# Optimization experiments

Hardware: AMD Instinct MI355X
Metric: run time of the kernel (lower is better)

Reference implementation:

```python
import jax, jax.numpy as jnp
import numpy as np

N_HEADS = 4
M = 16            # n_points (neighbors kept per voxel)
DIST = 4          # manhattan distance threshold
D_MODEL = 128
D_FFN = 256
D_CHL = 64
GRID = 96         # spatial_shape per axis
LN_EPS = 1e-5
BN_EPS = 1e-3


def setup_inputs() -> dict:
    key = jax.random.key(0)
    ks = jax.random.split(key, 24)
    N = 8192
    w = lambda k, s: jax.random.normal(k, s, jnp.float32) * 0.02
    z = lambda d: jnp.zeros((d,), jnp.float32)
    o = lambda d: jnp.ones((d,), jnp.float32)
    return {
        "features": jax.random.normal(ks[0], (N, D_CHL), jnp.float32),
        "coords": jax.random.randint(ks[1], (N, 3), 0, GRID, jnp.int32),
        "pe_w1": w(ks[2], (3, D_MODEL // 2)), "pe_b1": z(D_MODEL // 2),
        "pe_w2": w(ks[3], (D_MODEL // 2, D_MODEL)), "pe_b2": z(D_MODEL),
        "in_w": w(ks[4], (D_CHL, D_MODEL)), "in_b": z(D_MODEL),
        "q_w": w(ks[5], (D_MODEL, D_MODEL)), "q_b": z(D_MODEL),
        "k_w": w(ks[6], (D_MODEL, D_MODEL)), "k_b": z(D_MODEL),
        "v_w": w(ks[7], (D_MODEL, D_MODEL)), "v_b": z(D_MODEL),
        "o_w": w(ks[8], (D_MODEL, D_MODEL)), "o_b": z(D_MODEL),
        "n1_g": o(D_MODEL), "n1_b": z(D_MODEL),
        "l1_w": w(ks[9], (D_MODEL, D_FFN)), "l1_b": z(D_FFN),
        "l2_w": w(ks[10], (D_FFN, D_MODEL)), "l2_b": z(D_MODEL),
        "n3_g": o(D_MODEL), "n3_b": z(D_MODEL),
        "fu_w": w(ks[11], (D_MODEL + D_CHL, D_CHL)), "fu_b": z(D_CHL),
        "bn_g": o(D_CHL), "bn_b": z(D_CHL),
    }


def _layernorm(x, g, b):
    mu = jnp.mean(x, -1, keepdims=True)
    var = jnp.mean(jnp.square(x - mu), -1, keepdims=True)
    return (x - mu) * jax.lax.rsqrt(var + LN_EPS) * g + b


def reference(features, coords, pe_w1, pe_b1, pe_w2, pe_b2, in_w, in_b,
              q_w, q_b, k_w, k_b, v_w, v_b, o_w, o_b, n1_g, n1_b,
              l1_w, l1_b, l2_w, l2_b, n3_g, n3_b, fu_w, fu_b, bn_g, bn_b):
    N = features.shape[0]
    hd = D_MODEL // N_HEADS
    ci = coords.astype(jnp.float32)
    # input projection + dynamic learnable positional encoding
    src = features @ in_w + in_b
    vc = ci / (GRID - 1.0)
    src = src + (jax.nn.relu(vc @ pe_w1 + pe_b1) @ pe_w2 + pe_b2)
    # pairwise manhattan distances; accumulate per coordinate to avoid [N,N,3]
    dist = jnp.zeros((N, N), jnp.float32)
    for d in range(3):
        dist = dist + jnp.abs(ci[:, d, None] - ci[None, :, d])
    dist = jnp.where(dist <= DIST, dist, jnp.inf)
    neg_top, idx = jax.lax.top_k(-dist, M)          # [N, M]
    valid = neg_top != -jnp.inf
    # gather neighbor features; invalid slots are zero (as in torch)
    nb = jnp.where(valid[:, :, None], src[jnp.where(valid, idx, 0)], 0.0)  # [N,M,D]
    # cross-attention: query is neighbor 0 (self). NOTE: faithful raw .view
    # reshape of [N,M,D] -> [N,H,M,hd] (interleaves neighbor/head axes as torch does)
    q = (nb[:, :1] @ q_w + q_b).reshape(N, N_HEADS, 1, hd)
    k = (nb @ k_w + k_b).reshape(N, N_HEADS, M, hd)
    v = (nb @ v_w + v_b).reshape(N, N_HEADS, M, hd)
    scores = jnp.einsum('nhqd,nhkd->nhqk', q, k) / jnp.sqrt(jnp.float32(D_MODEL))
    attn = jax.nn.softmax(scores, axis=-1)
    head_out = jnp.einsum('nhqk,nhkd->nhqd', attn, v).reshape(N, D_MODEL)
    out = head_out @ o_w + o_b
    tgt = _layernorm(src + out, n1_g, n1_b)
    # FFN
    tgt2 = jax.nn.relu(tgt @ l1_w + l1_b) @ l2_w + l2_b
    tgt = _layernorm(tgt + tgt2, n3_g, n3_b)
    # EnhancedFusion: concat -> linear -> batchnorm (train-mode stats) -> relu
    fused = jnp.concatenate([features, tgt], axis=1) @ fu_w + fu_b
    mu = jnp.mean(fused, 0)
    var = jnp.var(fused, 0)
    fused = (fused - mu) * jax.lax.rsqrt(var + BN_EPS) * bn_g + bn_b
    return jax.nn.relu(fused)
```

## Files before the change

### kernel.cpp

```cpp
#include <hip/hip_runtime.h>

#define DEVFN __device__ __forceinline__

DEVFN float relu(float x) { return x < 0.f ? 0.f : x; }

__global__ void k0_zero_cst(float* __restrict__ p, int n)
{
    int i = blockIdx.x * 256 + threadIdx.x;
    if (i < n) p[i] = 0.f;
}

__global__ __launch_bounds__(256) void k1_src_cst(
    const float* __restrict__ features, const int* __restrict__ coords,
    const float* __restrict__ pe_w1, const float* __restrict__ pe_b1,
    const float* __restrict__ pe_w2, const float* __restrict__ pe_b2,
    const float* __restrict__ in_w, const float* __restrict__ in_b,
    float* __restrict__ src, int* __restrict__ packed)
{
    __shared__ float sF[512];
    __shared__ float sH[512];
    __shared__ int   sC[24];
    const int tid = threadIdx.x;
    const int r0 = blockIdx.x * 8;
    if (tid < 24) sC[tid] = coords[r0 * 3 + tid];
    for (int i = tid; i < 512; i += 256) sF[i] = features[r0 * 64 + i];
    __syncthreads();
    for (int i = tid; i < 512; i += 256) {
        int r = i >> 6, t = i & 63;
        float v0 = sC[r * 3 + 0] * (1.f / 95.f);
        float v1 = sC[r * 3 + 1] * (1.f / 95.f);
        float v2 = sC[r * 3 + 2] * (1.f / 95.f);
        float h = v0 * pe_w1[t] + v1 * pe_w1[64 + t] + v2 * pe_w1[128 + t] + pe_b1[t];
        sH[i] = relu(h);
    }
    __syncthreads();
    const int c = tid & 127, rh = tid >> 7;
    float acc[4];
    const float base = in_b[c] + pe_b2[c];
#pragma unroll
    for (int r = 0; r < 4; ++r) acc[r] = base;
    for (int j = 0; j < 64; ++j) {
        float w1 = in_w[j * 128 + c];
        float w2 = pe_w2[j * 128 + c];
#pragma unroll
        for (int r = 0; r < 4; ++r) {
            int rr = rh * 4 + r;
            acc[r] += sF[rr * 64 + j] * w1 + sH[rr * 64 + j] * w2;
        }
    }
#pragma unroll
    for (int r = 0; r < 4; ++r) src[(r0 + rh * 4 + r) * 128 + c] = acc[r];
    if (tid < 8)
        packed[r0 + tid] = sC[tid * 3] | (sC[tid * 3 + 1] << 8) | (sC[tid * 3 + 2] << 16);
}

__global__ __launch_bounds__(256) void k2_nbr_cst(
    const int* __restrict__ packed, int* __restrict__ nbr, int N)
{
    __shared__ int pc[8192];
    __shared__ int cnt[16];
    __shared__ int lst[16 * 64];
    __shared__ int outL[256];
    const int tid = threadIdx.x;
    for (int i = tid; i < N; i += 256) pc[i] = packed[i];
    if (tid < 16) cnt[tid] = 0;
    outL[tid] = -1;
    __syncthreads();
    const int q0 = blockIdx.x * 16;
    int qx[16], qy[16], qz[16];
#pragma unroll
    for (int q = 0; q < 16; ++q) {
        int p = pc[q0 + q];
        qx[q] = p & 255; qy[q] = (p >> 8) & 255; qz[q] = p >> 16;
    }
    for (int cd = tid; cd < N; cd += 256) {
        int p = pc[cd];
        int cx = p & 255, cy = (p >> 8) & 255, cz = p >> 16;
#pragma unroll
        for (int q = 0; q < 16; ++q) {
            int dx = cx - qx[q]; dx = dx < 0 ? -dx : dx;
            int dy = cy - qy[q]; dy = dy < 0 ? -dy : dy;
            int dz = cz - qz[q]; dz = dz < 0 ? -dz : dz;
            int d = dx + dy + dz;
            if (d <= 4) {
                int s = atomicAdd(&cnt[q], 1);
                if (s < 64) lst[q * 64 + s] = (d << 13) | cd;
            }
        }
    }
    __syncthreads();
    {
        const int q = tid >> 4, t = tid & 15;
        int n = cnt[q]; if (n > 64) n = 64;
        for (int e = t; e < n; e += 16) {
            int key = lst[q * 64 + e];
            int rank = 0;
            for (int j = 0; j < n; ++j) rank += (lst[q * 64 + j] < key) ? 1 : 0;
            if (rank < 16) outL[q * 16 + rank] = key & 8191;
        }
    }
    __syncthreads();
    {
        const int q = tid >> 4, t = tid & 15;
        nbr[(q0 + q) * 16 + t] = outL[q * 16 + t];
    }
}

__global__ __launch_bounds__(256) void k3_qkv_cst(
    const float* __restrict__ src,
    const float* __restrict__ q_w, const float* __restrict__ k_w,
    const float* __restrict__ v_w,
    float* __restrict__ qs, float* __restrict__ ks, float* __restrict__ vs)
{
    __shared__ float S[1024];
    const int tid = threadIdx.x;
    const int r0 = blockIdx.x * 8;
    const int which = blockIdx.y;
    const float* __restrict__ w = (which == 0) ? q_w : (which == 1) ? k_w : v_w;
    float* __restrict__ out = (which == 0) ? qs : (which == 1) ? ks : vs;
    for (int i = tid; i < 1024; i += 256) S[i] = src[r0 * 128 + i];
    __syncthreads();
    const int c = tid & 127, rh = tid >> 7;
    float acc[4];
#pragma unroll
    for (int r = 0; r < 4; ++r) acc[r] = 0.f;
    for (int k4 = 0; k4 < 32; ++k4) {
        float w0 = w[(k4 * 4 + 0) * 128 + c];
        float w1 = w[(k4 * 4 + 1) * 128 + c];
        float w2 = w[(k4 * 4 + 2) * 128 + c];
        float w3 = w[(k4 * 4 + 3) * 128 + c];
#pragma unroll
        for (int r = 0; r < 4; ++r) {
            float4 s = *(const float4*)(&S[(rh * 4 + r) * 128 + k4 * 4]);
            acc[r] += s.x * w0 + s.y * w1 + s.z * w2 + s.w * w3;
        }
    }
#pragma unroll
    for (int r = 0; r < 4; ++r) out[(r0 + rh * 4 + r) * 128 + c] = acc[r];
}

DEVFN void ln_rows8(float* Cb, const float* __restrict__ g,
                    const float* __restrict__ b, int tid)
{
    const int r = tid >> 5, l = tid & 31;
    float x[4]; float s = 0.f, s2 = 0.f;
#pragma unroll
    for (int i = 0; i < 4; ++i) {
        x[i] = Cb[r * 128 + l * 4 + i];
        s += x[i]; s2 += x[i] * x[i];
    }
#pragma unroll
    for (int o = 1; o < 32; o <<= 1) { s += __shfl_xor(s, o); s2 += __shfl_xor(s2, o); }
    float mu = s * (1.f / 128.f);
    float var = s2 * (1.f / 128.f) - mu * mu;
    float rstd = rsqrtf(var + 1e-5f);
#pragma unroll
    for (int i = 0; i < 4; ++i) {
        int cc = l * 4 + i;
        Cb[r * 128 + cc] = (x[i] - mu) * rstd * g[cc] + b[cc];
    }
}

__global__ __launch_bounds__(256) void k4_main_cst(
    const float* __restrict__ features, const float* __restrict__ src,
    const float* __restrict__ qs, const float* __restrict__ ks, const float* __restrict__ vs,
    const int* __restrict__ nbr,
    const float* __restrict__ q_b, const float* __restrict__ k_b,
    const float* __restrict__ v_b,
    const float* __restrict__ o_w, const float* __restrict__ o_b,
    const float* __restrict__ n1_g, const float* __restrict__ n1_b,
    const float* __restrict__ l1_w, const float* __restrict__ l1_b,
    const float* __restrict__ l2_w, const float* __restrict__ l2_b,
    const float* __restrict__ n3_g, const float* __restrict__ n3_b,
    const float* __restrict__ fu_w, const float* __restrict__ fu_b,
    float* __restrict__ fused, float* __restrict__ bnSum, float* __restrict__ bnSq)
{
    __shared__ float A[1024];
    __shared__ float Bt[1024];
    __shared__ float C[1024];
    __shared__ float Q[1024];
    __shared__ float H[2048];
    __shared__ float SC[512];
    __shared__ float F[512];
    __shared__ __align__(16) float bK[128], bV[128];
    __shared__ float bQ[128];
    __shared__ int idxL[128];
    const int tid = threadIdx.x;
    const int r0 = blockIdx.x * 8;

    for (int i = tid; i < 1024; i += 256) A[i] = src[r0 * 128 + i];
    for (int i = tid; i < 512; i += 256) F[i] = features[r0 * 64 + i];
    if (tid < 128) {
        idxL[tid] = nbr[r0 * 16 + tid];
        bQ[tid] = q_b[tid]; bK[tid] = k_b[tid]; bV[tid] = v_b[tid];
    }
    __syncthreads();
    for (int i = tid; i < 1024; i += 256) {
        int r = i >> 7, c = i & 127;
        int i0 = idxL[r * 16];
        Q[i] = (i0 < 0 ? 0.f : qs[i0 * 128 + c]) + bQ[c];
    }
    __syncthreads();

    const int ar = tid >> 5, ah = (tid >> 3) & 3, ag = tid & 7;
    {
#pragma unroll
        for (int jj = 0; jj < 2; ++jj) {
            int j = ag + jj * 8;
            int j4 = j >> 2, ch = j & 3;
            int id = idxL[ar * 16 + ah * 4 + j4];
            float s = 0.f;
#pragma unroll
            for (int c4 = 0; c4 < 8; ++c4) {
                float4 qv = *(const float4*)(&Q[ar * 128 + ah * 32 + c4 * 4]);
                float4 kb = *(const float4*)(&bK[ch * 32 + c4 * 4]);
                float4 kv = make_float4(0.f, 0.f, 0.f, 0.f);
                if (id >= 0) kv = *(const float4*)(ks + id * 128 + ch * 32 + c4 * 4);
                s += qv.x * (kv.x + kb.x) + qv.y * (kv.y + kb.y)
                   + qv.z * (kv.z + kb.z) + qv.w * (kv.w + kb.w);
            }
            SC[ar * 64 + ah * 16 + j] = s * 0.08838834764831845f;
        }
    }
    __syncthreads();

    {
        float p[16];
        float mx = -3.4e38f;
#pragma unroll
        for (int j = 0; j < 16; ++j) { p[j] = SC[ar * 64 + ah * 16 + j]; mx = fmaxf(mx, p[j]); }
        float sum = 0.f;
#pragma unroll
        for (int j = 0; j < 16; ++j) { p[j] = __expf(p[j] - mx); sum += p[j]; }
        float inv = 1.f / sum;
        float4 acc = make_float4(0.f, 0.f, 0.f, 0.f);
#pragma unroll
        for (int j = 0; j < 16; ++j) {
            int j4 = j >> 2, ch = j & 3;
            int id = idxL[ar * 16 + ah * 4 + j4];
            float4 vb = *(const float4*)(&bV[ch * 32 + ag * 4]);
            float4 vv = make_float4(0.f, 0.f, 0.f, 0.f);
            if (id >= 0) vv = *(const float4*)(vs + id * 128 + ch * 32 + ag * 4);
            float w = p[j] * inv;
            acc.x += w * (vv.x + vb.x); acc.y += w * (vv.y + vb.y);
            acc.z += w * (vv.z + vb.z); acc.w += w * (vv.w + vb.w);
        }
        *(float4*)(&Bt[ar * 128 + ah * 32 + ag * 4]) = acc;
    }
    __syncthreads();

    {
        const int c = tid & 127, rh = tid >> 7;
        float acc[4];
        const float ob = o_b[c];
#pragma unroll
        for (int r = 0; r < 4; ++r) acc[r] = ob;
        for (int k4 = 0; k4 < 32; ++k4) {
            float w0 = o_w[(k4 * 4 + 0) * 128 + c];
            float w1 = o_w[(k4 * 4 + 1) * 128 + c];
            float w2 = o_w[(k4 * 4 + 2) * 128 + c];
            float w3 = o_w[(k4 * 4 + 3) * 128 + c];
#pragma unroll
            for (int r = 0; r < 4; ++r) {
                float4 t = *(const float4*)(&Bt[(rh * 4 + r) * 128 + k4 * 4]);
                acc[r] += t.x * w0 + t.y * w1 + t.z * w2 + t.w * w3;
            }
        }
#pragma unroll
        for (int r = 0; r < 4; ++r) {
            int row = rh * 4 + r;
            C[row * 128 + c] = A[row * 128 + c] + acc[r];
        }
    }
    __syncthreads();
    ln_rows8(C, n1_g, n1_b, tid);
    __syncthreads();

    {
        const int f = tid;
        float acc[8];
#pragma unroll
        for (int r = 0; r < 8; ++r) acc[r] = 0.f;
        for (int k4 = 0; k4 < 32; ++k4) {
            float w0 = l1_w[(k4 * 4 + 0) * 256 + f];
            float w1 = l1_w[(k4 * 4 + 1) * 256 + f];
            float w2 = l1_w[(k4 * 4 + 2) * 256 + f];
            float w3 = l1_w[(k4 * 4 + 3) * 256 + f];
#pragma unroll
            for (int r = 0; r < 8; ++r) {
                float4 t = *(const float4*)(&C[r * 128 + k4 * 4]);
                acc[r] += t.x * w0 + t.y * w1 + t.z * w2 + t.w * w3;
            }
        }
        const float bb = l1_b[f];
#pragma unroll
        for (int r = 0; r < 8; ++r) H[r * 256 + f] = relu(acc[r] + bb);
    }
    __syncthreads();

    {
        const int c = tid & 127, rh = tid >> 7;
        float acc[4];
        const float lb = l2_b[c];
#pragma unroll
        for (int r = 0; r < 4; ++r) acc[r] = lb;
        for (int k4 = 0; k4 < 64; ++k4) {
            float w0 = l2_w[(k4 * 4 + 0) * 128 + c];
            float w1 = l2_w[(k4 * 4 + 1) * 128 + c];
            float w2 = l2_w[(k4 * 4 + 2) * 128 + c];
            float w3 = l2_w[(k4 * 4 + 3) * 128 + c];
#pragma unroll
            for (int r = 0; r < 4; ++r) {
                float4 t = *(const float4*)(&H[(rh * 4 + r) * 256 + k4 * 4]);
                acc[r] += t.x * w0 + t.y * w1 + t.z * w2 + t.w * w3;
            }
        }
#pragma unroll
        for (int r = 0; r < 4; ++r) {
            int row = rh * 4 + r;
            C[row * 128 + c] += acc[r];
        }
    }
    __syncthreads();
    ln_rows8(C, n3_g, n3_b, tid);
    __syncthreads();

    {
        const int c = tid & 63, rg = tid >> 6;
        float acc[2];
        const float fb = fu_b[c];
#pragma unroll
        for (int r = 0; r < 2; ++r) acc[r] = fb;
        for (int j4 = 0; j4 < 16; ++j4) {
            float w0 = fu_w[(j4 * 4 + 0) * 64 + c];
            float w1 = fu_w[(j4 * 4 + 1) * 64 + c];
            float w2 = fu_w[(j4 * 4 + 2) * 64 + c];
            float w3 = fu_w[(j4 * 4 + 3) * 64 + c];
#pragma unroll
            for (int r = 0; r < 2; ++r) {
                float4 t = *(const float4*)(&F[(rg * 2 + r) * 64 + j4 * 4]);
                acc[r] += t.x * w0 + t.y * w1 + t.z * w2 + t.w * w3;
            }
        }
        for (int j4 = 0; j4 < 32; ++j4) {
            float w0 = fu_w[(64 + j4 * 4 + 0) * 64 + c];
            float w1 = fu_w[(64 + j4 * 4 + 1) * 64 + c];
            float w2 = fu_w[(64 + j4 * 4 + 2) * 64 + c];
            float w3 = fu_w[(64 + j4 * 4 + 3) * 64 + c];
#pragma unroll
            for (int r = 0; r < 2; ++r) {
                float4 t = *(const float4*)(&C[(rg * 2 + r) * 128 + j4 * 4]);
                acc[r] += t.x * w0 + t.y * w1 + t.z * w2 + t.w * w3;
            }
        }
#pragma unroll
        for (int r = 0; r < 2; ++r) {
            int row = rg * 2 + r;
            float v = acc[r];
            fused[(r0 + row) * 64 + c] = v;
            H[row * 64 + c] = v;
        }
    }
    __syncthreads();
    if (tid < 64) {
        float s = 0.f, s2 = 0.f;
#pragma unroll
        for (int r = 0; r < 8; ++r) { float x = H[r * 64 + tid]; s += x; s2 += x * x; }
        atomicAdd(&bnSum[tid], s);
        atomicAdd(&bnSq[tid], s2);
    }
}

__global__ __launch_bounds__(256) void k5_bn_cst(
    const float* __restrict__ fused, const float* __restrict__ bnSum,
    const float* __restrict__ bnSq,
    const float* __restrict__ g, const float* __restrict__ b,
    float* __restrict__ out, int N)
{
    const int total = N * 64;
    const float invN = 1.f / (float)N;
    for (int i = blockIdx.x * 256 + threadIdx.x; i < total; i += gridDim.x * 256) {
        int c = i & 63;
        float mu = bnSum[c] * invN;
        float var = bnSq[c] * invN - mu * mu;
        float x = fused[i];
        float y = (x - mu) * rsqrtf(var + 1e-3f) * g[c] + b[c];
        out[i] = relu(y);
    }
}

extern "C" void kernel_launch(void* const* d_in, const int* in_sizes, int n_in,
                              void* d_out, int out_size, void* d_ws, size_t ws_size,
                              hipStream_t stream)
{
    const float* features = (const float*)d_in[0];
    const int*   coords   = (const int*)d_in[1];
    const float* pe_w1 = (const float*)d_in[2];
    const float* pe_b1 = (const float*)d_in[3];
    const float* pe_w2 = (const float*)d_in[4];
    const float* pe_b2 = (const float*)d_in[5];
    const float* in_w  = (const float*)d_in[6];
    const float* in_b  = (const float*)d_in[7];
    const float* q_w   = (const float*)d_in[8];
    const float* q_b   = (const float*)d_in[9];
    const float* k_w   = (const float*)d_in[10];
    const float* k_b   = (const float*)d_in[11];
    const float* v_w   = (const float*)d_in[12];
    const float* v_b   = (const float*)d_in[13];
    const float* o_w   = (const float*)d_in[14];
    const float* o_b   = (const float*)d_in[15];
    const float* n1_g  = (const float*)d_in[16];
    const float* n1_b  = (const float*)d_in[17];
    const float* l1_w  = (const float*)d_in[18];
    const float* l1_b  = (const float*)d_in[19];
    const float* l2_w  = (const float*)d_in[20];
    const float* l2_b  = (const float*)d_in[21];
    const float* n3_g  = (const float*)d_in[22];
    const float* n3_b  = (const float*)d_in[23];
    const float* fu_w  = (const float*)d_in[24];
    const float* fu_b  = (const float*)d_in[25];
    const float* bn_g  = (const float*)d_in[26];
    const float* bn_b  = (const float*)d_in[27];

    const int N = in_sizes[0] / 64;

    float* src   = (float*)d_ws;
    float* qs    = src + (size_t)N * 128;
    float* ks    = qs  + (size_t)N * 128;
    float* vs    = ks  + (size_t)N * 128;
    float* fused = vs  + (size_t)N * 128;
    int*   packed = (int*)(fused + (size_t)N * 64);
    int*   nbr    = packed + N;
    float* bnSum  = (float*)(nbr + (size_t)N * 16);
    float* bnSq   = bnSum + 64;

    k0_zero_cst<<<1, 256, 0, stream>>>(bnSum, 128);
    k1_src_cst<<<N / 8, 256, 0, stream>>>(features, coords, pe_w1, pe_b1, pe_w2, pe_b2,
                                          in_w, in_b, src, packed);
    k2_nbr_cst<<<N / 16, 256, 0, stream>>>(packed, nbr, N);
    k3_qkv_cst<<<dim3(N / 8, 3), 256, 0, stream>>>(src, q_w, k_w, v_w, qs, ks, vs);
    k4_main_cst<<<N / 8, 256, 0, stream>>>(features, src, qs, ks, vs, nbr,
                                           q_b, k_b, v_b, o_w, o_b, n1_g, n1_b,
                                           l1_w, l1_b, l2_w, l2_b, n3_g, n3_b,
                                           fu_w, fu_b, fused, bnSum, bnSq);
    k5_bn_cst<<<512, 256, 0, stream>>>(fused, bnSum, bnSq, bn_g, bn_b,
                                       (float*)d_out, N);
}
```

Before: 235.9 us.

## Fuse src projection with QKV projection and fold BN zeroing into neighbor kernel

Merges the input/positional-encoding projection kernel with the Q/K/V projection kernel, so src stays in shared memory and is not reloaded from global memory. The separate zeroing kernel for the batch-norm accumulators is removed, and that zeroing now happens in block 0 of the neighbor-search kernel. Weight-loop pointers are hoisted and loops are given unroll-4 pragmas throughout. Together these cut two launches and one global round-trip of src. In exchange, the fused kernel does three times the per-block work with only N/8 blocks, where QKV previously used a 3x grid, which lowers parallelism.

```diff
diff --git a/kernel.cpp b/kernel.cpp
--- a/kernel.cpp
+++ b/kernel.cpp
@@ -4,21 +4,19 @@
 
 DEVFN float relu(float x) { return x < 0.f ? 0.f : x; }
 
-__global__ void k0_zero_cst(float* __restrict__ p, int n)
-{
-    int i = blockIdx.x * 256 + threadIdx.x;
-    if (i < n) p[i] = 0.f;
-}
-
-__global__ __launch_bounds__(256) void k1_src_cst(
+__global__ __launch_bounds__(256) void k13_src_qkv_cst(
     const float* __restrict__ features, const int* __restrict__ coords,
     const float* __restrict__ pe_w1, const float* __restrict__ pe_b1,
     const float* __restrict__ pe_w2, const float* __restrict__ pe_b2,
     const float* __restrict__ in_w, const float* __restrict__ in_b,
-    float* __restrict__ src, int* __restrict__ packed)
+    const float* __restrict__ q_w, const float* __restrict__ k_w,
+    const float* __restrict__ v_w,
+    float* __restrict__ src, int* __restrict__ packed,
+    float* __restrict__ qs, float* __restrict__ ks, float* __restrict__ vs)
 {
     __shared__ float sF[512];
     __shared__ float sH[512];
+    __shared__ float S[1024];
     __shared__ int   sC[24];
     const int tid = threadIdx.x;
     const int r0 = blockIdx.x * 8;
@@ -35,33 +33,67 @@
     }
     __syncthreads();
     const int c = tid & 127, rh = tid >> 7;
-    float acc[4];
-    const float base = in_b[c] + pe_b2[c];
-#pragma unroll
-    for (int r = 0; r < 4; ++r) acc[r] = base;
-    for (int j = 0; j < 64; ++j) {
-        float w1 = in_w[j * 128 + c];
-        float w2 = pe_w2[j * 128 + c];
+    {
+        float acc[4];
+        const float base = in_b[c] + pe_b2[c];
+#pragma unroll
+        for (int r = 0; r < 4; ++r) acc[r] = base;
+        const float* w1p = in_w + c;
+        const float* w2p = pe_w2 + c;
+#pragma unroll 4
+        for (int j = 0; j < 64; ++j) {
+            float w1 = w1p[j * 128];
+            float w2 = w2p[j * 128];
+#pragma unroll
+            for (int r = 0; r < 4; ++r) {
+                int rr = rh * 4 + r;
+                acc[r] += sF[rr * 64 + j] * w1 + sH[rr * 64 + j] * w2;
+            }
+        }
 #pragma unroll
         for (int r = 0; r < 4; ++r) {
-            int rr = rh * 4 + r;
-            acc[r] += sF[rr * 64 + j] * w1 + sH[rr * 64 + j] * w2;
-        }
-    }
-#pragma unroll
-    for (int r = 0; r < 4; ++r) src[(r0 + rh * 4 + r) * 128 + c] = acc[r];
-    if (tid < 8)
-        packed[r0 + tid] = sC[tid * 3] | (sC[tid * 3 + 1] << 8) | (sC[tid * 3 + 2] << 16);
+            src[(r0 + rh * 4 + r) * 128 + c] = acc[r];
+            S[(rh * 4 + r) * 128 + c] = acc[r];
+        }
+        if (tid < 8)
+            packed[r0 + tid] = sC[tid * 3] | (sC[tid * 3 + 1] << 8) | (sC[tid * 3 + 2] << 16);
+    }
+    __syncthreads();
+#pragma unroll
+    for (int which = 0; which < 3; ++which) {
+        const float* __restrict__ w = (which == 0) ? q_w : (which == 1) ? k_w : v_w;
+        float* __restrict__ out = (which == 0) ? qs : (which == 1) ? ks : vs;
+        float acc[4];
+#pragma unroll
+        for (int r = 0; r < 4; ++r) acc[r] = 0.f;
+        const float* wp = w + c;
+#pragma unroll 4
+        for (int k4 = 0; k4 < 32; ++k4) {
+            float w0 = wp[(k4 * 4 + 0) * 128];
+            float w1 = wp[(k4 * 4 + 1) * 128];
+            float w2 = wp[(k4 * 4 + 2) * 128];
+            float w3 = wp[(k4 * 4 + 3) * 128];
+#pragma unroll
+            for (int r = 0; r < 4; ++r) {
+                float4 s = *(const float4*)(&S[(rh * 4 + r) * 128 + k4 * 4]);
+                acc[r] += s.x * w0 + s.y * w1 + s.z * w2 + s.w * w3;
+            }
+        }
+#pragma unroll
+        for (int r = 0; r < 4; ++r) out[(r0 + rh * 4 + r) * 128 + c] = acc[r];
+    }
 }
 
 __global__ __launch_bounds__(256) void k2_nbr_cst(
-    const int* __restrict__ packed, int* __restrict__ nbr, int N)
+    const int* __restrict__ packed, int* __restrict__ nbr,
+    float* __restrict__ bnAcc, int N)
 {
     __shared__ int pc[8192];
     __shared__ int cnt[16];
     __shared__ int lst[16 * 64];
     __shared__ int outL[256];
     const int tid = threadIdx.x;
+    if (blockIdx.x == 0 && tid < 128) bnAcc[tid] = 0.f;
     for (int i = tid; i < N; i += 256) pc[i] = packed[i];
     if (tid < 16) cnt[tid] = 0;
     outL[tid] = -1;
@@ -104,39 +136,6 @@
         const int q = tid >> 4, t = tid & 15;
         nbr[(q0 + q) * 16 + t] = outL[q * 16 + t];
     }
-}
-
-__global__ __launch_bounds__(256) void k3_qkv_cst(
-    const float* __restrict__ src,
-    const float* __restrict__ q_w, const float* __restrict__ k_w,
-    const float* __restrict__ v_w,
-    float* __restrict__ qs, float* __restrict__ ks, float* __restrict__ vs)
-{
-    __shared__ float S[1024];
-    const int tid = threadIdx.x;
-    const int r0 = blockIdx.x * 8;
-    const int which = blockIdx.y;
-    const float* __restrict__ w = (which == 0) ? q_w : (which == 1) ? k_w : v_w;
-    float* __restrict__ out = (which == 0) ? qs : (which == 1) ? ks : vs;
-    for (int i = tid; i < 1024; i += 256) S[i] = src[r0 * 128 + i];
-    __syncthreads();
-    const int c = tid & 127, rh = tid >> 7;
-    float acc[4];
-#pragma unroll
-    for (int r = 0; r < 4; ++r) acc[r] = 0.f;
-    for (int k4 = 0; k4 < 32; ++k4) {
-        float w0 = w[(k4 * 4 + 0) * 128 + c];
-        float w1 = w[(k4 * 4 + 1) * 128 + c];
-        float w2 = w[(k4 * 4 + 2) * 128 + c];
-        float w3 = w[(k4 * 4 + 3) * 128 + c];
-#pragma unroll
-        for (int r = 0; r < 4; ++r) {
-            float4 s = *(const float4*)(&S[(rh * 4 + r) * 128 + k4 * 4]);
-            acc[r] += s.x * w0 + s.y * w1 + s.z * w2 + s.w * w3;
-        }
-    }
-#pragma unroll
-    for (int r = 0; r < 4; ++r) out[(r0 + rh * 4 + r) * 128 + c] = acc[r];
 }
 
 DEVFN void ln_rows8(float* Cb, const float* __restrict__ g,
@@ -255,11 +254,13 @@
         const float ob = o_b[c];
 #pragma unroll
         for (int r = 0; r < 4; ++r) acc[r] = ob;
+        const float* wp = o_w + c;
+#pragma unroll 4
         for (int k4 = 0; k4 < 32; ++k4) {
-            float w0 = o_w[(k4 * 4 + 0) * 128 + c];
-            float w1 = o_w[(k4 * 4 + 1) * 128 + c];
-            float w2 = o_w[(k4 * 4 + 2) * 128 + c];
-            float w3 = o_w[(k4 * 4 + 3) * 128 + c];
+            float w0 = wp[(k4 * 4 + 0) * 128];
+            float w1 = wp[(k4 * 4 + 1) * 128];
+            float w2 = wp[(k4 * 4 + 2) * 128];
+            float w3 = wp[(k4 * 4 + 3) * 128];
 #pragma unroll
             for (int r = 0; r < 4; ++r) {
                 float4 t = *(const float4*)(&Bt[(rh * 4 + r) * 128 + k4 * 4]);
@@ -281,11 +282,13 @@
         float acc[8];
 #pragma unroll
         for (int r = 0; r < 8; ++r) acc[r] = 0.f;
+        const float* wp = l1_w + f;
+#pragma unroll 4
         for (int k4 = 0; k4 < 32; ++k4) {
-            float w0 = l1_w[(k4 * 4 + 0) * 256 + f];
-            float w1 = l1_w[(k4 * 4 + 1) * 256 + f];
-            float w2 = l1_w[(k4 * 4 + 2) * 256 + f];
-            float w3 = l1_w[(k4 * 4 + 3) * 256 + f];
+            float w0 = wp[(k4 * 4 + 0) * 256];
+            float w1 = wp[(k4 * 4 + 1) * 256];
+            float w2 = wp[(k4 * 4 + 2) * 256];
+            float w3 = wp[(k4 * 4 + 3) * 256];
 #pragma unroll
             for (int r = 0; r < 8; ++r) {
                 float4 t = *(const float4*)(&C[r * 128 + k4 * 4]);
@@ -304,11 +307,13 @@
         const float lb = l2_b[c];
 #pragma unroll
         for (int r = 0; r < 4; ++r) acc[r] = lb;
+        const float* wp = l2_w + c;
+#pragma unroll 4
         for (int k4 = 0; k4 < 64; ++k4) {
-            float w0 = l2_w[(k4 * 4 + 0) * 128 + c];
-            float w1 = l2_w[(k4 * 4 + 1) * 128 + c];
-            float w2 = l2_w[(k4 * 4 + 2) * 128 + c];
-            float w3 = l2_w[(k4 * 4 + 3) * 128 + c];
+            float w0 = wp[(k4 * 4 + 0) * 128];
+            float w1 = wp[(k4 * 4 + 1) * 128];
+            float w2 = wp[(k4 * 4 + 2) * 128];
+            float w3 = wp[(k4 * 4 + 3) * 128];
 #pragma unroll
             for (int r = 0; r < 4; ++r) {
                 float4 t = *(const float4*)(&H[(rh * 4 + r) * 256 + k4 * 4]);
@@ -331,22 +336,26 @@
         const float fb = fu_b[c];
 #pragma unroll
         for (int r = 0; r < 2; ++r) acc[r] = fb;
+        const float* wp = fu_w + c;
+#pragma unroll 4
         for (int j4 = 0; j4 < 16; ++j4) {
-            float w0 = fu_w[(j4 * 4 + 0) * 64 + c];
-            float w1 = fu_w[(j4 * 4 + 1) * 64 + c];
-            float w2 = fu_w[(j4 * 4 + 2) * 64 + c];
-            float w3 = fu_w[(j4 * 4 + 3) * 64 + c];
+            float w0 = wp[(j4 * 4 + 0) * 64];
+            float w1 = wp[(j4 * 4 + 1) * 64];
+            float w2 = wp[(j4 * 4 + 2) * 64];
+            float w3 = wp[(j4 * 4 + 3) * 64];
 #pragma unroll
             for (int r = 0; r < 2; ++r) {
                 float4 t = *(const float4*)(&F[(rg * 2 + r) * 64 + j4 * 4]);
                 acc[r] += t.x * w0 + t.y * w1 + t.z * w2 + t.w * w3;
             }
         }
+        const float* wp2 = fu_w + 64 * 64 + c;
+#pragma unroll 4
         for (int j4 = 0; j4 < 32; ++j4) {
-            float w0 = fu_w[(64 + j4 * 4 + 0) * 64 + c];
-            float w1 = fu_w[(64 + j4 * 4 + 1) * 64 + c];
-            float w2 = fu_w[(64 + j4 * 4 + 2) * 64 + c];
-            float w3 = fu_w[(64 + j4 * 4 + 3) * 64 + c];
+            float w0 = wp2[(j4 * 4 + 0) * 64];
+            float w1 = wp2[(j4 * 4 + 1) * 64];
+            float w2 = wp2[(j4 * 4 + 2) * 64];
+            float w3 = wp2[(j4 * 4 + 3) * 64];
 #pragma unroll
             for (int r = 0; r < 2; ++r) {
                 float4 t = *(const float4*)(&C[(rg * 2 + r) * 128 + j4 * 4]);
@@ -434,11 +443,11 @@
     float* bnSum  = (float*)(nbr + (size_t)N * 16);
     float* bnSq   = bnSum + 64;
 
-    k0_zero_cst<<<1, 256, 0, stream>>>(bnSum, 128);
-    k1_src_cst<<<N / 8, 256, 0, stream>>>(features, coords, pe_w1, pe_b1, pe_w2, pe_b2,
-                                          in_w, in_b, src, packed);
-    k2_nbr_cst<<<N / 16, 256, 0, stream>>>(packed, nbr, N);
-    k3_qkv_cst<<<dim3(N / 8, 3), 256, 0, stream>>>(src, q_w, k_w, v_w, qs, ks, vs);
+    k13_src_qkv_cst<<<N / 8, 256, 0, stream>>>(features, coords, pe_w1, pe_b1,
+                                               pe_w2, pe_b2, in_w, in_b,
+                                               q_w, k_w, v_w,
+                                               src, packed, qs, ks, vs);
+    k2_nbr_cst<<<N / 16, 256, 0, stream>>>(packed, nbr, bnSum, N);
     k4_main_cst<<<N / 8, 256, 0, stream>>>(features, src, qs, ks, vs, nbr,
                                            q_b, k_b, v_b, o_w, o_b, n1_g, n1_b,
                                            l1_w, l1_b, l2_w, l2_b, n3_g, n3_b,
```

After: 242.8 us. +2.9%, slower.

## Fuse src projection, QKV, neighbor search and BN zeroing into one kernel

Applied to the files above, without the earlier changes.

Merges the zeroing kernel, the src/positional-encoding kernel, the neighbor search kernel and the QKV projection into one launch. Src blocks and neighbor-search blocks run side by side, split by block index. The neighbor search now reads coords straight from global memory instead of staging packed coords in 32KB of LDS. QKV is computed from src kept in shared memory, which removes the src re-read and three separate launches. The cost is a larger LDS footprint per block across both roles, more registers for the three accumulators, and uncoalesced strided coord reads in the search loop.

```diff
diff --git a/kernel.cpp b/kernel.cpp
--- a/kernel.cpp
+++ b/kernel.cpp
@@ -4,23 +4,77 @@
 
 DEVFN float relu(float x) { return x < 0.f ? 0.f : x; }
 
-__global__ void k0_zero_cst(float* __restrict__ p, int n)
-{
-    int i = blockIdx.x * 256 + threadIdx.x;
-    if (i < n) p[i] = 0.f;
-}
-
-__global__ __launch_bounds__(256) void k1_src_cst(
+__global__ __launch_bounds__(256) void ka_pre_cst(
     const float* __restrict__ features, const int* __restrict__ coords,
     const float* __restrict__ pe_w1, const float* __restrict__ pe_b1,
     const float* __restrict__ pe_w2, const float* __restrict__ pe_b2,
     const float* __restrict__ in_w, const float* __restrict__ in_b,
-    float* __restrict__ src, int* __restrict__ packed)
+    const float* __restrict__ q_w, const float* __restrict__ k_w,
+    const float* __restrict__ v_w,
+    float* __restrict__ src,
+    float* __restrict__ qs, float* __restrict__ ks, float* __restrict__ vs,
+    int* __restrict__ nbr, float* __restrict__ bnAcc, int N)
 {
     __shared__ float sF[512];
     __shared__ float sH[512];
+    __shared__ float S[1024];
     __shared__ int   sC[24];
+    __shared__ int cnt[16];
+    __shared__ int lst[16 * 64];
+    __shared__ int outL[256];
+
     const int tid = threadIdx.x;
+    const int nSrcBlocks = N / 8;
+
+    if ((int)blockIdx.x >= nSrcBlocks) {
+        const int nb = blockIdx.x - nSrcBlocks;
+        const int q0 = nb * 16;
+        if (nb == 0 && tid < 128) bnAcc[tid] = 0.f;
+        if (tid < 16) cnt[tid] = 0;
+        outL[tid] = -1;
+        __syncthreads();
+        int qx[16], qy[16], qz[16];
+#pragma unroll
+        for (int q = 0; q < 16; ++q) {
+            qx[q] = coords[(q0 + q) * 3 + 0];
+            qy[q] = coords[(q0 + q) * 3 + 1];
+            qz[q] = coords[(q0 + q) * 3 + 2];
+        }
+        for (int cd = tid; cd < N; cd += 256) {
+            int cx = coords[cd * 3 + 0];
+            int cy = coords[cd * 3 + 1];
+            int cz = coords[cd * 3 + 2];
+#pragma unroll
+            for (int q = 0; q < 16; ++q) {
+                int dx = cx - qx[q]; dx = dx < 0 ? -dx : dx;
+                int dy = cy - qy[q]; dy = dy < 0 ? -dy : dy;
+                int dz = cz - qz[q]; dz = dz < 0 ? -dz : dz;
+                int d = dx + dy + dz;
+                if (d <= 4) {
+                    int s = atomicAdd(&cnt[q], 1);
+                    if (s < 64) lst[q * 64 + s] = (d << 13) | cd;
+                }
+            }
+        }
+        __syncthreads();
+        {
+            const int q = tid >> 4, t = tid & 15;
+            int n = cnt[q]; if (n > 64) n = 64;
+            for (int e = t; e < n; e += 16) {
+                int key = lst[q * 64 + e];
+                int rank = 0;
+                for (int j = 0; j < n; ++j) rank += (lst[q * 64 + j] < key) ? 1 : 0;
+                if (rank < 16) outL[q * 16 + rank] = key & 8191;
+            }
+        }
+        __syncthreads();
+        {
+            const int q = tid >> 4, t = tid & 15;
+            nbr[(q0 + q) * 16 + t] = outL[q * 16 + t];
+        }
+        return;
+    }
+
     const int r0 = blockIdx.x * 8;
     if (tid < 24) sC[tid] = coords[r0 * 3 + tid];
     for (int i = tid; i < 512; i += 256) sF[i] = features[r0 * 64 + i];
@@ -35,108 +89,59 @@
     }
     __syncthreads();
     const int c = tid & 127, rh = tid >> 7;
-    float acc[4];
-    const float base = in_b[c] + pe_b2[c];
-#pragma unroll
-    for (int r = 0; r < 4; ++r) acc[r] = base;
-    for (int j = 0; j < 64; ++j) {
-        float w1 = in_w[j * 128 + c];
-        float w2 = pe_w2[j * 128 + c];
+    {
+        float acc[4];
+        const float base = in_b[c] + pe_b2[c];
+#pragma unroll
+        for (int r = 0; r < 4; ++r) acc[r] = base;
+        for (int j = 0; j < 64; ++j) {
+            float w1 = in_w[j * 128 + c];
+            float w2 = pe_w2[j * 128 + c];
+#pragma unroll
+            for (int r = 0; r < 4; ++r) {
+                int rr = rh * 4 + r;
+                acc[r] += sF[rr * 64 + j] * w1 + sH[rr * 64 + j] * w2;
+            }
+        }
 #pragma unroll
         for (int r = 0; r < 4; ++r) {
-            int rr = rh * 4 + r;
-            acc[r] += sF[rr * 64 + j] * w1 + sH[rr * 64 + j] * w2;
-        }
-    }
-#pragma unroll
-    for (int r = 0; r < 4; ++r) src[(r0 + rh * 4 + r) * 128 + c] = acc[r];
-    if (tid < 8)
-        packed[r0 + tid] = sC[tid * 3] | (sC[tid * 3 + 1] << 8) | (sC[tid * 3 + 2] << 16);
-}
-
-__global__ __launch_bounds__(256) void k2_nbr_cst(
-    const int* __restrict__ packed, int* __restrict__ nbr, int N)
-{
-    __shared__ int pc[8192];
-    __shared__ int cnt[16];
-    __shared__ int lst[16 * 64];
-    __shared__ int outL[256];
-    const int tid = threadIdx.x;
-    for (int i = tid; i < N; i += 256) pc[i] = packed[i];
-    if (tid < 16) cnt[tid] = 0;
-    outL[tid] = -1;
-    __syncthreads();
-    const int q0 = blockIdx.x * 16;
-    int qx[16], qy[16], qz[16];
-#pragma unroll
-    for (int q = 0; q < 16; ++q) {
-        int p = pc[q0 + q];
-        qx[q] = p & 255; qy[q] = (p >> 8) & 255; qz[q] = p >> 16;
-    }
-    for (int cd = tid; cd < N; cd += 256) {
-        int p = pc[cd];
-        int cx = p & 255, cy = (p >> 8) & 255, cz = p >> 16;
-#pragma unroll
-        for (int q = 0; q < 16; ++q) {
-            int dx = cx - qx[q]; dx = dx < 0 ? -dx : dx;
-            int dy = cy - qy[q]; dy = dy < 0 ? -dy : dy;
-            int dz = cz - qz[q]; dz = dz < 0 ? -dz : dz;
-            int d = dx + dy + dz;
-            if (d <= 4) {
-                int s = atomicAdd(&cnt[q], 1);
-                if (s < 64) lst[q * 64 + s] = (d << 13) | cd;
-            }
-        }
-    }
-    __syncthreads();
-    {
-        const int q = tid >> 4, t = tid & 15;
-        int n = cnt[q]; if (n > 64) n = 64;
-        for (int e = t; e < n; e += 16) {
-            int key = lst[q * 64 + e];
-            int rank = 0;
-            for (int j = 0; j < n; ++j) rank += (lst[q * 64 + j] < key) ? 1 : 0;
-            if (rank < 16) outL[q * 16 + rank] = key & 8191;
-        }
-    }
-    __syncthreads();
-    {
-        const int q = tid >> 4, t = tid & 15;
-        nbr[(q0 + q) * 16 + t] = outL[q * 16 + t];
-    }
-}
-
-__global__ __launch_bounds__(256) void k3_qkv_cst(
-    const float* __restrict__ src,
-    const float* __restrict__ q_w, const float* __restrict__ k_w,
-    const float* __restrict__ v_w,
-    float* __restrict__ qs, float* __restrict__ ks, float* __restrict__ vs)
-{
-    __shared__ float S[1024];
-    const int tid = threadIdx.x;
-    const int r0 = blockIdx.x * 8;
-    const int which = blockIdx.y;
-    const float* __restrict__ w = (which == 0) ? q_w : (which == 1) ? k_w : v_w;
-    float* __restrict__ out = (which == 0) ? qs : (which == 1) ? ks : vs;
-    for (int i = tid; i < 1024; i += 256) S[i] = src[r0 * 128 + i];
-    __syncthreads();
-    const int c = tid & 127, rh = tid >> 7;
-    float acc[4];
-#pragma unroll
-    for (int r = 0; r < 4; ++r) acc[r] = 0.f;
-    for (int k4 = 0; k4 < 32; ++k4) {
-        float w0 = w[(k4 * 4 + 0) * 128 + c];
-        float w1 = w[(k4 * 4 + 1) * 128 + c];
-        float w2 = w[(k4 * 4 + 2) * 128 + c];
-        float w3 = w[(k4 * 4 + 3) * 128 + c];
+            src[(r0 + rh * 4 + r) * 128 + c] = acc[r];
+            S[(rh * 4 + r) * 128 + c] = acc[r];
+        }
+    }
+    __syncthreads();
+    {
+        float aq[4], ak[4], av[4];
+#pragma unroll
+        for (int r = 0; r < 4; ++r) { aq[r] = 0.f; ak[r] = 0.f; av[r] = 0.f; }
+        for (int k4 = 0; k4 < 32; ++k4) {
+            float wq0 = q_w[(k4 * 4 + 0) * 128 + c];
+            float wq1 = q_w[(k4 * 4 + 1) * 128 + c];
+            float wq2 = q_w[(k4 * 4 + 2) * 128 + c];
+            float wq3 = q_w[(k4 * 4 + 3) * 128 + c];
+            float wk0 = k_w[(k4 * 4 + 0) * 128 + c];
+            float wk1 = k_w[(k4 * 4 + 1) * 128 + c];
+            float wk2 = k_w[(k4 * 4 + 2) * 128 + c];
+            float wk3 = k_w[(k4 * 4 + 3) * 128 + c];
+            float wv0 = v_w[(k4 * 4 + 0) * 128 + c];
+            float wv1 = v_w[(k4 * 4 + 1) * 128 + c];
+            float wv2 = v_w[(k4 * 4 + 2) * 128 + c];
+            float wv3 = v_w[(k4 * 4 + 3) * 128 + c];
+#pragma unroll
+            for (int r = 0; r < 4; ++r) {
+                float4 s = *(const float4*)(&S[(rh * 4 + r) * 128 + k4 * 4]);
+                aq[r] += s.x * wq0 + s.y * wq1 + s.z * wq2 + s.w * wq3;
+                ak[r] += s.x * wk0 + s.y * wk1 + s.z * wk2 + s.w * wk3;
+                av[r] += s.x * wv0 + s.y * wv1 + s.z * wv2 + s.w * wv3;
+            }
+        }
 #pragma unroll
         for (int r = 0; r < 4; ++r) {
-            float4 s = *(const float4*)(&S[(rh * 4 + r) * 128 + k4 * 4]);
-            acc[r] += s.x * w0 + s.y * w1 + s.z * w2 + s.w * w3;
-        }
-    }
-#pragma unroll
-    for (int r = 0; r < 4; ++r) out[(r0 + rh * 4 + r) * 128 + c] = acc[r];
+            qs[(r0 + rh * 4 + r) * 128 + c] = aq[r];
+            ks[(r0 + rh * 4 + r) * 128 + c] = ak[r];
+            vs[(r0 + rh * 4 + r) * 128 + c] = av[r];
+        }
+    }
 }
 
 DEVFN void ln_rows8(float* Cb, const float* __restrict__ g,
@@ -429,16 +434,14 @@
     float* ks    = qs  + (size_t)N * 128;
     float* vs    = ks  + (size_t)N * 128;
     float* fused = vs  + (size_t)N * 128;
-    int*   packed = (int*)(fused + (size_t)N * 64);
-    int*   nbr    = packed + N;
+    int*   nbr    = (int*)(fused + (size_t)N * 64);
     float* bnSum  = (float*)(nbr + (size_t)N * 16);
     float* bnSq   = bnSum + 64;
 
-    k0_zero_cst<<<1, 256, 0, stream>>>(bnSum, 128);
-    k1_src_cst<<<N / 8, 256, 0, stream>>>(features, coords, pe_w1, pe_b1, pe_w2, pe_b2,
-                                          in_w, in_b, src, packed);
-    k2_nbr_cst<<<N / 16, 256, 0, stream>>>(packed, nbr, N);
-    k3_qkv_cst<<<dim3(N / 8, 3), 256, 0, stream>>>(src, q_w, k_w, v_w, qs, ks, vs);
+    ka_pre_cst<<<N / 8 + N / 16, 256, 0, stream>>>(features, coords,
+                                                   pe_w1, pe_b1, pe_w2, pe_b2,
+                                                   in_w, in_b, q_w, k_w, v_w,
+                                                   src, qs, ks, vs, nbr, bnSum, N);
     k4_main_cst<<<N / 8, 256, 0, stream>>>(features, src, qs, ks, vs, nbr,
                                            q_b, k_b, v_b, o_w, o_b, n1_g, n1_b,
                                            l1_w, l1_b, l2_w, l2_b, n3_g, n3_b,
```

New measurement: 228.1 us. 3.3% less time.
